# Kernel tuning notes

Hardware: AMD Instinct MI355X
Metric: run time of the kernel (lower is better)

## Reference

```python
import jax, jax.numpy as jnp
import numpy as np

SIGMA_INIT = 1000.0


def setup_inputs() -> dict:
    key = jax.random.key(0)
    k1, k2, k3 = jax.random.split(key, 3)
    B, M, D, S = 1024, 209, 12288, 2
    input_data = jax.random.normal(k1, (B, D), dtype=jnp.float32)
    center = jax.random.normal(k2, (M, D), dtype=jnp.float32)
    sigma = SIGMA_INIT * jnp.ones((M,), dtype=jnp.float32)
    W = 50.0 * jax.random.normal(k3, (S, M), dtype=jnp.float32)
    b = jnp.zeros((S,), dtype=jnp.float32)
    return {"input_data": input_data, "center": center, "sigma": sigma, "W": W, "b": b}


def reference(input_data, center, sigma, W, b):
    # Euclidean distance ||x_i - c_j|| via GEMM expansion (avoids [B,M,D] diff tensor)
    x2 = jnp.sum(input_data * input_data, axis=1, keepdims=True)        # [B,1]
    c2 = jnp.sum(center * center, axis=1)[None, :]                      # [1,M]
    d2 = x2 + c2 - 2.0 * (input_data @ center.T)                        # [B,M]
    dist = jnp.sqrt(jnp.maximum(d2, 0.0))
    # Note: original divides the (non-squared) norm by sigma^2, then exp(-.)
    radial = jnp.exp(-dist / (sigma * sigma)[None, :])                  # [B,M]
    return radial @ W.T + b                                             # [B,S]
```

## Files before the change

kernel.cpp:

```cpp
#include <hip/hip_runtime.h>
#include <hip/hip_bf16.h>
#include <stdint.h>

#define B_SZ 1024
#define M_SZ 209
#define D_SZ 12288
#define S_SZ 2

#define BT   64
#define MT   224
#define NCT  14
#define KC   48
#define KCH  (D_SZ / KC)
#define BK   64
#define NIT  (KCH / BK)
#define LDX  72

#define WS_DOT_OFF 1280

typedef __attribute__((ext_vector_type(8))) short short8;
typedef __attribute__((ext_vector_type(4))) float floatx4;

__device__ __forceinline__ uint32_t pk2(float lo, float hi) {
    union { __hip_bfloat162 h; uint32_t u; } cv;
    cv.h = __float22bfloat162_rn(float2{lo, hi});
    return cv.u;
}

__global__ __launch_bounds__(256, 3) void rbf_main(
    const float* __restrict__ x, const float* __restrict__ c,
    float* __restrict__ dot, float* __restrict__ xx, float* __restrict__ cc,
    int atomic_mode)
{
    __shared__ unsigned short sx[BT * LDX];
    __shared__ unsigned short sc[MT * LDX];

    const int t      = threadIdx.x;
    const int kchunk = blockIdx.x;
    const int bchunk = blockIdx.y;
    const int wave   = t >> 6;
    const int lane   = t & 63;
    const int quad   = lane >> 4;
    const int mrow   = lane & 15;

    floatx4 acc[NCT];
    const floatx4 zero4 = {0.f, 0.f, 0.f, 0.f};
#pragma unroll
    for (int i = 0; i < NCT; ++i) acc[i] = zero4;

    const int r     = t >> 2;
    const int cbase = (t & 3) * 16;

    const float* xp = x + (size_t)(bchunk * BT + r) * D_SZ + kchunk * KCH + cbase;
    const float* cp = c + (size_t)r * D_SZ + kchunk * KCH + cbase;
    const bool do_cc = (bchunk == 0);

    float sxx = 0.f;
    float scc[4] = {0.f, 0.f, 0.f, 0.f};

    for (int it = 0; it < NIT; ++it) {
        {
            float4 v0 = *(const float4*)(xp + 0);
            float4 v1 = *(const float4*)(xp + 4);
            float4 v2 = *(const float4*)(xp + 8);
            float4 v3 = *(const float4*)(xp + 12);
            sxx += v0.x*v0.x + v0.y*v0.y + v0.z*v0.z + v0.w*v0.w
                 + v1.x*v1.x + v1.y*v1.y + v1.z*v1.z + v1.w*v1.w
                 + v2.x*v2.x + v2.y*v2.y + v2.z*v2.z + v2.w*v2.w
                 + v3.x*v3.x + v3.y*v3.y + v3.z*v3.z + v3.w*v3.w;
            uint4 w0 = { pk2(v0.x,v0.y), pk2(v0.z,v0.w), pk2(v1.x,v1.y), pk2(v1.z,v1.w) };
            uint4 w1 = { pk2(v2.x,v2.y), pk2(v2.z,v2.w), pk2(v3.x,v3.y), pk2(v3.z,v3.w) };
            *(uint4*)(&sx[r * LDX + cbase])     = w0;
            *(uint4*)(&sx[r * LDX + cbase + 8]) = w1;
        }
#pragma unroll
        for (int rb = 0; rb < 4; ++rb) {
            const int crow = rb * 64 + r;
            if (rb < 3 || r < 32) {
                const bool valid = crow < M_SZ;
                const float* p = cp + (size_t)rb * 64 * D_SZ;
                float4 v0, v1, v2, v3;
                if (valid) {
                    v0 = *(const float4*)(p + 0);  v1 = *(const float4*)(p + 4);
                    v2 = *(const float4*)(p + 8);  v3 = *(const float4*)(p + 12);
                } else {
                    v0 = v1 = v2 = v3 = make_float4(0.f, 0.f, 0.f, 0.f);
                }
                if (do_cc && valid) {
                    scc[rb] += v0.x*v0.x + v0.y*v0.y + v0.z*v0.z + v0.w*v0.w
                             + v1.x*v1.x + v1.y*v1.y + v1.z*v1.z + v1.w*v1.w
                             + v2.x*v2.x + v2.y*v2.y + v2.z*v2.z + v2.w*v2.w
                             + v3.x*v3.x + v3.y*v3.y + v3.z*v3.z + v3.w*v3.w;
                }
                uint4 w0 = { pk2(v0.x,v0.y), pk2(v0.z,v0.w), pk2(v1.x,v1.y), pk2(v1.z,v1.w) };
                uint4 w1 = { pk2(v2.x,v2.y), pk2(v2.z,v2.w), pk2(v3.x,v3.y), pk2(v3.z,v3.w) };
                *(uint4*)(&sc[crow * LDX + cbase])     = w0;
                *(uint4*)(&sc[crow * LDX + cbase + 8]) = w1;
            }
        }
        __syncthreads();

        const unsigned short* ax = &sx[(wave * 16 + mrow) * LDX + quad * 8];
        const unsigned short* bx = &sc[mrow * LDX + quad * 8];
#pragma unroll
        for (int k0 = 0; k0 < BK; k0 += 32) {
            short8 a = *(const short8*)(ax + k0);
#pragma unroll
            for (int ct = 0; ct < NCT; ++ct) {
                short8 b = *(const short8*)(bx + ct * 16 * LDX + k0);
                acc[ct] = __builtin_amdgcn_mfma_f32_16x16x32_bf16(a, b, acc[ct], 0, 0, 0);
            }
        }
        __syncthreads();
        xp += BK;
        cp += BK;
    }

    float* dst = atomic_mode ? dot : dot + (size_t)kchunk * B_SZ * M_SZ;
    const int gi0 = bchunk * BT + wave * 16 + quad * 4;
#pragma unroll
    for (int ct = 0; ct < NCT; ++ct) {
        const int gj = ct * 16 + mrow;
        if (gj < M_SZ) {
#pragma unroll
            for (int rg = 0; rg < 4; ++rg) {
                const size_t idx = (size_t)(gi0 + rg) * M_SZ + gj;
                if (atomic_mode) atomicAdd(&dst[idx], acc[ct][rg]);
                else             dst[idx] = acc[ct][rg];
            }
        }
    }

    sxx += __shfl_down(sxx, 2);
    sxx += __shfl_down(sxx, 1);
    if ((t & 3) == 0) atomicAdd(&xx[bchunk * BT + r], sxx);

    if (do_cc) {
#pragma unroll
        for (int rb = 0; rb < 4; ++rb) {
            float s = scc[rb];
            s += __shfl_down(s, 2);
            s += __shfl_down(s, 1);
            const int crow = rb * 64 + r;
            if ((t & 3) == 0 && crow < M_SZ) atomicAdd(&cc[crow], s);
        }
    }
}

template <int NKC>
__global__ __launch_bounds__(256) void rbf_fin(
    const float* __restrict__ dot, const float* __restrict__ xx,
    const float* __restrict__ cc, const float* __restrict__ sigma,
    const float* __restrict__ W, const float* __restrict__ bias,
    float* __restrict__ out)
{
    const int wave = threadIdx.x >> 6, lane = threadIdx.x & 63;
    const int i = blockIdx.x * 4 + wave;
    const float xxi = xx[i];
    float a0 = 0.f, a1 = 0.f;
    for (int j = lane; j < M_SZ; j += 64) {
        float s = 0.f;
#pragma unroll
        for (int k = 0; k < NKC; ++k)
            s += dot[(size_t)k * B_SZ * M_SZ + (size_t)i * M_SZ + j];
        float d2 = fmaxf(xxi + cc[j] - 2.f * s, 0.f);
        float sg = sigma[j];
        float rad = __expf(-sqrtf(d2) / (sg * sg));
        a0 += rad * W[j];
        a1 += rad * W[M_SZ + j];
    }
#pragma unroll
    for (int off = 32; off > 0; off >>= 1) {
        a0 += __shfl_down(a0, off);
        a1 += __shfl_down(a1, off);
    }
    if (lane == 0) {
        out[i * 2 + 0] = a0 + bias[0];
        out[i * 2 + 1] = a1 + bias[1];
    }
}

extern "C" void kernel_launch(void* const* d_in, const int* in_sizes, int n_in,
                              void* d_out, int out_size, void* d_ws, size_t ws_size,
                              hipStream_t stream)
{
    const float* x     = (const float*)d_in[0];
    const float* c     = (const float*)d_in[1];
    const float* sigma = (const float*)d_in[2];
    const float* W     = (const float*)d_in[3];
    const float* bias  = (const float*)d_in[4];
    float* out = (float*)d_out;

    float* xx  = (float*)d_ws;
    float* cc  = xx + B_SZ;
    float* dot = (float*)d_ws + WS_DOT_OFF;

    const size_t slab_bytes = ((size_t)WS_DOT_OFF + (size_t)KC * B_SZ * M_SZ) * 4;
    const int atomic_mode = (ws_size < slab_bytes) ? 1 : 0;

    const size_t zero_bytes = atomic_mode
        ? ((size_t)WS_DOT_OFF + (size_t)B_SZ * M_SZ) * 4
        : (size_t)WS_DOT_OFF * 4;
    hipMemsetAsync(d_ws, 0, zero_bytes, stream);

    rbf_main<<<dim3(KC, B_SZ / BT), 256, 0, stream>>>(x, c, dot, xx, cc, atomic_mode);
    if (atomic_mode)
        rbf_fin<1><<<B_SZ / 4, 256, 0, stream>>>(dot, xx, cc, sigma, W, bias, out);
    else
        rbf_fin<KC><<<B_SZ / 4, 256, 0, stream>>>(dot, xx, cc, sigma, W, bias, out);
}
```

Measured before the change: 125.2 us.

## Split center dimension across a third grid axis to double block count

Each block now processes half the centers (112 instead of 224 padded), with a new grid z-dimension of 2, halving per-block accumulators and shared memory. Launch bounds are raised to 6 blocks per CU to exploit the lower register/LDS footprint and improve occupancy and latency hiding. The cost is that each x tile is loaded and converted twice (once per center half), increasing global traffic for x, while the squared-norm accumulation for x is restricted to the first half.

```diff
diff --git a/kernel.cpp b/kernel.cpp
--- a/kernel.cpp
+++ b/kernel.cpp
@@ -8,8 +8,9 @@
 #define S_SZ 2
 
 #define BT   64
-#define MT   224
-#define NCT  14
+#define MS   2
+#define MTH  112
+#define NCT  7
 #define KC   48
 #define KCH  (D_SZ / KC)
 #define BK   64
@@ -27,17 +28,26 @@
     return cv.u;
 }
 
-__global__ __launch_bounds__(256, 3) void rbf_main(
+__device__ __forceinline__ float sq16(const float4& a, const float4& b,
+                                      const float4& c, const float4& d) {
+    return a.x*a.x + a.y*a.y + a.z*a.z + a.w*a.w
+         + b.x*b.x + b.y*b.y + b.z*b.z + b.w*b.w
+         + c.x*c.x + c.y*c.y + c.z*c.z + c.w*c.w
+         + d.x*d.x + d.y*d.y + d.z*d.z + d.w*d.w;
+}
+
+__global__ __launch_bounds__(256, 6) void rbf_main(
     const float* __restrict__ x, const float* __restrict__ c,
     float* __restrict__ dot, float* __restrict__ xx, float* __restrict__ cc,
     int atomic_mode)
 {
     __shared__ unsigned short sx[BT * LDX];
-    __shared__ unsigned short sc[MT * LDX];
+    __shared__ unsigned short sc[MTH * LDX];
 
     const int t      = threadIdx.x;
     const int kchunk = blockIdx.x;
     const int bchunk = blockIdx.y;
+    const int mchunk = blockIdx.z;
     const int wave   = t >> 6;
     const int lane   = t & 63;
     const int quad   = lane >> 4;
@@ -51,12 +61,12 @@
     const int r     = t >> 2;
     const int cbase = (t & 3) * 16;
 
-    const float* xp = x + (size_t)(bchunk * BT + r) * D_SZ + kchunk * KCH + cbase;
-    const float* cp = c + (size_t)r * D_SZ + kchunk * KCH + cbase;
+    const float* xp  = x + (size_t)(bchunk * BT + r) * D_SZ + kchunk * KCH + cbase;
+    const float* cp0 = c + (size_t)mchunk * MTH * D_SZ + kchunk * KCH + cbase;
     const bool do_cc = (bchunk == 0);
 
     float sxx = 0.f;
-    float scc[4] = {0.f, 0.f, 0.f, 0.f};
+    float scc[2] = {0.f, 0.f};
 
     for (int it = 0; it < NIT; ++it) {
         {
@@ -64,21 +74,19 @@
             float4 v1 = *(const float4*)(xp + 4);
             float4 v2 = *(const float4*)(xp + 8);
             float4 v3 = *(const float4*)(xp + 12);
-            sxx += v0.x*v0.x + v0.y*v0.y + v0.z*v0.z + v0.w*v0.w
-                 + v1.x*v1.x + v1.y*v1.y + v1.z*v1.z + v1.w*v1.w
-                 + v2.x*v2.x + v2.y*v2.y + v2.z*v2.z + v2.w*v2.w
-                 + v3.x*v3.x + v3.y*v3.y + v3.z*v3.z + v3.w*v3.w;
+            sxx += sq16(v0, v1, v2, v3);
             uint4 w0 = { pk2(v0.x,v0.y), pk2(v0.z,v0.w), pk2(v1.x,v1.y), pk2(v1.z,v1.w) };
             uint4 w1 = { pk2(v2.x,v2.y), pk2(v2.z,v2.w), pk2(v3.x,v3.y), pk2(v3.z,v3.w) };
             *(uint4*)(&sx[r * LDX + cbase])     = w0;
             *(uint4*)(&sx[r * LDX + cbase + 8]) = w1;
         }
 #pragma unroll
-        for (int rb = 0; rb < 4; ++rb) {
+        for (int rb = 0; rb < 2; ++rb) {
             const int crow = rb * 64 + r;
-            if (rb < 3 || r < 32) {
-                const bool valid = crow < M_SZ;
-                const float* p = cp + (size_t)rb * 64 * D_SZ;
+            if (rb == 0 || r < 48) {
+                const int  grow  = mchunk * MTH + crow;
+                const bool valid = grow < M_SZ;
+                const float* p = cp0 + (size_t)crow * D_SZ;
                 float4 v0, v1, v2, v3;
                 if (valid) {
                     v0 = *(const float4*)(p + 0);  v1 = *(const float4*)(p + 4);
@@ -86,12 +94,7 @@
                 } else {
                     v0 = v1 = v2 = v3 = make_float4(0.f, 0.f, 0.f, 0.f);
                 }
-                if (do_cc && valid) {
-                    scc[rb] += v0.x*v0.x + v0.y*v0.y + v0.z*v0.z + v0.w*v0.w
-                             + v1.x*v1.x + v1.y*v1.y + v1.z*v1.z + v1.w*v1.w
-                             + v2.x*v2.x + v2.y*v2.y + v2.z*v2.z + v2.w*v2.w
-                             + v3.x*v3.x + v3.y*v3.y + v3.z*v3.z + v3.w*v3.w;
-                }
+                if (do_cc && valid) scc[rb] += sq16(v0, v1, v2, v3);
                 uint4 w0 = { pk2(v0.x,v0.y), pk2(v0.z,v0.w), pk2(v1.x,v1.y), pk2(v1.z,v1.w) };
                 uint4 w1 = { pk2(v2.x,v2.y), pk2(v2.z,v2.w), pk2(v3.x,v3.y), pk2(v3.z,v3.w) };
                 *(uint4*)(&sc[crow * LDX + cbase])     = w0;
@@ -113,14 +116,14 @@
         }
         __syncthreads();
         xp += BK;
-        cp += BK;
+        cp0 += BK;
     }
 
     float* dst = atomic_mode ? dot : dot + (size_t)kchunk * B_SZ * M_SZ;
     const int gi0 = bchunk * BT + wave * 16 + quad * 4;
 #pragma unroll
     for (int ct = 0; ct < NCT; ++ct) {
-        const int gj = ct * 16 + mrow;
+        const int gj = mchunk * MTH + ct * 16 + mrow;
         if (gj < M_SZ) {
 #pragma unroll
             for (int rg = 0; rg < 4; ++rg) {
@@ -131,18 +134,21 @@
         }
     }
 
-    sxx += __shfl_down(sxx, 2);
-    sxx += __shfl_down(sxx, 1);
-    if ((t & 3) == 0) atomicAdd(&xx[bchunk * BT + r], sxx);
+    if (mchunk == 0) {
+        sxx += __shfl_down(sxx, 2);
+        sxx += __shfl_down(sxx, 1);
+        if ((t & 3) == 0) atomicAdd(&xx[bchunk * BT + r], sxx);
+    }
 
     if (do_cc) {
 #pragma unroll
-        for (int rb = 0; rb < 4; ++rb) {
+        for (int rb = 0; rb < 2; ++rb) {
             float s = scc[rb];
             s += __shfl_down(s, 2);
             s += __shfl_down(s, 1);
-            const int crow = rb * 64 + r;
-            if ((t & 3) == 0 && crow < M_SZ) atomicAdd(&cc[crow], s);
+            const int grow = mchunk * MTH + rb * 64 + r;
+            if ((t & 3) == 0 && (rb == 0 || r < 48) && grow < M_SZ)
+                atomicAdd(&cc[grow], s);
         }
     }
 }
@@ -203,7 +209,7 @@
         : (size_t)WS_DOT_OFF * 4;
     hipMemsetAsync(d_ws, 0, zero_bytes, stream);
 
-    rbf_main<<<dim3(KC, B_SZ / BT), 256, 0, stream>>>(x, c, dot, xx, cc, atomic_mode);
+    rbf_main<<<dim3(KC, B_SZ / BT, MS), 256, 0, stream>>>(x, c, dot, xx, cc, atomic_mode);
     if (atomic_mode)
         rbf_fin<1><<<B_SZ / 4, 256, 0, stream>>>(dot, xx, cc, sigma, W, bias, out);
     else
```

Result: slower. 146.7 us (+17.2%).

## Pre-convert centers to bf16, async-load to swizzled LDS, store bf16 partials

Applied to the files above, without the earlier changes.

A new prep kernel converts the centers to a padded bf16 copy once and computes their squared norms. The main kernel then loads these tiles straight into LDS with global_load_lds, using an XOR-swizzled layout in place of padded rows to avoid bank conflicts. The per-K-chunk partial dot products are written as bf16 instead of fp32, and x norms go to per-chunk slots rather than atomics, which removes the memset and the atomic fallback path. This cuts the centers read per block, the fp32 convert work repeated across 16 batch chunks, and the slab write/read traffic. In exchange it adds a launch and loses accuracy by rounding partial sums to bf16 before the distance computation, which is large cancellation-sensitive.

```diff
diff --git a/kernel.cpp b/kernel.cpp
--- a/kernel.cpp
+++ b/kernel.cpp
@@ -4,19 +4,20 @@
 
 #define B_SZ 1024
 #define M_SZ 209
+#define MPAD 224
 #define D_SZ 12288
-#define S_SZ 2
-
-#define BT   64
-#define MT   224
-#define NCT  14
 #define KC   48
 #define KCH  (D_SZ / KC)
 #define BK   64
 #define NIT  (KCH / BK)
-#define LDX  72
-
-#define WS_DOT_OFF 1280
+#define NB   16
+#define BT   64
+#define NCT  14
+
+#define CBF_OFF  0u
+#define XXP_OFF  (MPAD * D_SZ * 2)
+#define CC_OFF   (XXP_OFF + B_SZ * KC * 4)
+#define SLAB_OFF (CC_OFF + 1024)
 
 typedef __attribute__((ext_vector_type(8))) short short8;
 typedef __attribute__((ext_vector_type(4))) float floatx4;
@@ -27,38 +28,81 @@
     return cv.u;
 }
 
+__device__ __forceinline__ void gload_lds16(const void* g, void* l) {
+    __builtin_amdgcn_global_load_lds(
+        (const __attribute__((address_space(1))) void*)g,
+        (__attribute__((address_space(3))) void*)l, 16, 0, 0);
+}
+
+__global__ __launch_bounds__(256) void rbf_prep(
+    const float* __restrict__ c, unsigned short* __restrict__ cbf,
+    float* __restrict__ cc)
+{
+    __shared__ float red[4];
+    const int j = blockIdx.x, t = threadIdx.x;
+    unsigned short* dst = cbf + (size_t)j * D_SZ;
+    float s = 0.f;
+    if (j < M_SZ) {
+        const float* src = c + (size_t)j * D_SZ;
+        for (int i = t * 4; i < D_SZ; i += 1024) {
+            float4 v = *(const float4*)(src + i);
+            s += v.x*v.x + v.y*v.y + v.z*v.z + v.w*v.w;
+            uint2 w = { pk2(v.x, v.y), pk2(v.z, v.w) };
+            *(uint2*)(dst + i) = w;
+        }
+    } else {
+        uint2 zz = {0u, 0u};
+        for (int i = t * 4; i < D_SZ; i += 1024) *(uint2*)(dst + i) = zz;
+    }
+#pragma unroll
+    for (int off = 32; off > 0; off >>= 1) s += __shfl_down(s, off);
+    if ((t & 63) == 0) red[t >> 6] = s;
+    __syncthreads();
+    if (t == 0 && j < M_SZ) cc[j] = red[0] + red[1] + red[2] + red[3];
+}
+
 __global__ __launch_bounds__(256, 3) void rbf_main(
-    const float* __restrict__ x, const float* __restrict__ c,
-    float* __restrict__ dot, float* __restrict__ xx, float* __restrict__ cc,
-    int atomic_mode)
-{
-    __shared__ unsigned short sx[BT * LDX];
-    __shared__ unsigned short sc[MT * LDX];
-
-    const int t      = threadIdx.x;
-    const int kchunk = blockIdx.x;
-    const int bchunk = blockIdx.y;
-    const int wave   = t >> 6;
-    const int lane   = t & 63;
-    const int quad   = lane >> 4;
-    const int mrow   = lane & 15;
+    const float* __restrict__ x, const unsigned short* __restrict__ cbf,
+    __hip_bfloat16* __restrict__ slab, float* __restrict__ xxp)
+{
+    __shared__ unsigned short sx[BT * BK];
+    __shared__ unsigned short sc[MPAD * BK];
+
+    const int t    = threadIdx.x;
+    const int k    = blockIdx.x;
+    const int b    = blockIdx.y;
+    const int wave = t >> 6, lane = t & 63;
+    const int quad = lane >> 4, mrow = lane & 15;
+    const int m3   = mrow & 7;
 
     floatx4 acc[NCT];
-    const floatx4 zero4 = {0.f, 0.f, 0.f, 0.f};
-#pragma unroll
-    for (int i = 0; i < NCT; ++i) acc[i] = zero4;
-
-    const int r     = t >> 2;
-    const int cbase = (t & 3) * 16;
-
-    const float* xp = x + (size_t)(bchunk * BT + r) * D_SZ + kchunk * KCH + cbase;
-    const float* cp = c + (size_t)r * D_SZ + kchunk * KCH + cbase;
-    const bool do_cc = (bchunk == 0);
+    const floatx4 z4 = {0.f, 0.f, 0.f, 0.f};
+#pragma unroll
+    for (int i = 0; i < NCT; ++i) acc[i] = z4;
+
+    const int r  = t >> 2;
+    const int c0 = (t & 3) * 2;
+    const float* xp = x + (size_t)(b * BT + r) * D_SZ + (size_t)k * KCH + (t & 3) * 16;
+    unsigned short* xw0 = &sx[r * BK + ((c0    ) ^ (r & 7)) * 8];
+    unsigned short* xw1 = &sx[r * BK + ((c0 + 1) ^ (r & 7)) * 8];
+
+    const int lr8 = lane >> 3, lc8 = lane & 7;
+    const unsigned short* cpb = cbf + (size_t)lr8 * D_SZ + (size_t)k * KCH
+                              + (size_t)((lc8 ^ lr8) * 8);
+
+    const unsigned short* ax0 = &sx[(wave * 16 + mrow) * BK + ((quad    ) ^ m3) * 8];
+    const unsigned short* ax1 = &sx[(wave * 16 + mrow) * BK + ((quad + 4) ^ m3) * 8];
+    const unsigned short* bx0 = &sc[mrow * BK + ((quad    ) ^ m3) * 8];
+    const unsigned short* bx1 = &sc[mrow * BK + ((quad + 4) ^ m3) * 8];
 
     float sxx = 0.f;
-    float scc[4] = {0.f, 0.f, 0.f, 0.f};
 
     for (int it = 0; it < NIT; ++it) {
+#pragma unroll
+        for (int j = 0; j < 7; ++j) {
+            const int cr = wave * 7 + j;
+            gload_lds16(cpb + (size_t)cr * 8 * D_SZ + it * BK, &sc[cr * 512]);
+        }
         {
             float4 v0 = *(const float4*)(xp + 0);
             float4 v1 = *(const float4*)(xp + 4);
@@ -70,99 +114,62 @@
                  + v3.x*v3.x + v3.y*v3.y + v3.z*v3.z + v3.w*v3.w;
             uint4 w0 = { pk2(v0.x,v0.y), pk2(v0.z,v0.w), pk2(v1.x,v1.y), pk2(v1.z,v1.w) };
             uint4 w1 = { pk2(v2.x,v2.y), pk2(v2.z,v2.w), pk2(v3.x,v3.y), pk2(v3.z,v3.w) };
-            *(uint4*)(&sx[r * LDX + cbase])     = w0;
-            *(uint4*)(&sx[r * LDX + cbase + 8]) = w1;
-        }
-#pragma unroll
-        for (int rb = 0; rb < 4; ++rb) {
-            const int crow = rb * 64 + r;
-            if (rb < 3 || r < 32) {
-                const bool valid = crow < M_SZ;
-                const float* p = cp + (size_t)rb * 64 * D_SZ;
-                float4 v0, v1, v2, v3;
-                if (valid) {
-                    v0 = *(const float4*)(p + 0);  v1 = *(const float4*)(p + 4);
-                    v2 = *(const float4*)(p + 8);  v3 = *(const float4*)(p + 12);
-                } else {
-                    v0 = v1 = v2 = v3 = make_float4(0.f, 0.f, 0.f, 0.f);
-                }
-                if (do_cc && valid) {
-                    scc[rb] += v0.x*v0.x + v0.y*v0.y + v0.z*v0.z + v0.w*v0.w
-                             + v1.x*v1.x + v1.y*v1.y + v1.z*v1.z + v1.w*v1.w
-                             + v2.x*v2.x + v2.y*v2.y + v2.z*v2.z + v2.w*v2.w
-                             + v3.x*v3.x + v3.y*v3.y + v3.z*v3.z + v3.w*v3.w;
-                }
-                uint4 w0 = { pk2(v0.x,v0.y), pk2(v0.z,v0.w), pk2(v1.x,v1.y), pk2(v1.z,v1.w) };
-                uint4 w1 = { pk2(v2.x,v2.y), pk2(v2.z,v2.w), pk2(v3.x,v3.y), pk2(v3.z,v3.w) };
-                *(uint4*)(&sc[crow * LDX + cbase])     = w0;
-                *(uint4*)(&sc[crow * LDX + cbase + 8]) = w1;
-            }
+            *(uint4*)xw0 = w0;
+            *(uint4*)xw1 = w1;
         }
         __syncthreads();
 
-        const unsigned short* ax = &sx[(wave * 16 + mrow) * LDX + quad * 8];
-        const unsigned short* bx = &sc[mrow * LDX + quad * 8];
-#pragma unroll
-        for (int k0 = 0; k0 < BK; k0 += 32) {
-            short8 a = *(const short8*)(ax + k0);
+#pragma unroll
+        for (int ks = 0; ks < 2; ++ks) {
+            short8 a = *(const short8*)(ks ? ax1 : ax0);
+            const unsigned short* bb = ks ? bx1 : bx0;
 #pragma unroll
             for (int ct = 0; ct < NCT; ++ct) {
-                short8 b = *(const short8*)(bx + ct * 16 * LDX + k0);
-                acc[ct] = __builtin_amdgcn_mfma_f32_16x16x32_bf16(a, b, acc[ct], 0, 0, 0);
+                short8 bf = *(const short8*)(bb + ct * 1024);
+                acc[ct] = __builtin_amdgcn_mfma_f32_16x16x32_bf16(a, bf, acc[ct], 0, 0, 0);
             }
         }
         __syncthreads();
         xp += BK;
-        cp += BK;
-    }
-
-    float* dst = atomic_mode ? dot : dot + (size_t)kchunk * B_SZ * M_SZ;
-    const int gi0 = bchunk * BT + wave * 16 + quad * 4;
+    }
+
+    __hip_bfloat16* sd = slab + (size_t)k * B_SZ * M_SZ;
+    const int gi0 = b * BT + wave * 16 + quad * 4;
 #pragma unroll
     for (int ct = 0; ct < NCT; ++ct) {
         const int gj = ct * 16 + mrow;
         if (gj < M_SZ) {
 #pragma unroll
-            for (int rg = 0; rg < 4; ++rg) {
-                const size_t idx = (size_t)(gi0 + rg) * M_SZ + gj;
-                if (atomic_mode) atomicAdd(&dst[idx], acc[ct][rg]);
-                else             dst[idx] = acc[ct][rg];
-            }
+            for (int rg = 0; rg < 4; ++rg)
+                sd[(size_t)(gi0 + rg) * M_SZ + gj] = __float2bfloat16(acc[ct][rg]);
         }
     }
 
     sxx += __shfl_down(sxx, 2);
     sxx += __shfl_down(sxx, 1);
-    if ((t & 3) == 0) atomicAdd(&xx[bchunk * BT + r], sxx);
-
-    if (do_cc) {
-#pragma unroll
-        for (int rb = 0; rb < 4; ++rb) {
-            float s = scc[rb];
-            s += __shfl_down(s, 2);
-            s += __shfl_down(s, 1);
-            const int crow = rb * 64 + r;
-            if ((t & 3) == 0 && crow < M_SZ) atomicAdd(&cc[crow], s);
-        }
-    }
-}
-
-template <int NKC>
+    if ((t & 3) == 0) xxp[(size_t)(b * BT + r) * KC + k] = sxx;
+}
+
 __global__ __launch_bounds__(256) void rbf_fin(
-    const float* __restrict__ dot, const float* __restrict__ xx,
+    const __hip_bfloat16* __restrict__ slab, const float* __restrict__ xxp,
     const float* __restrict__ cc, const float* __restrict__ sigma,
     const float* __restrict__ W, const float* __restrict__ bias,
     float* __restrict__ out)
 {
     const int wave = threadIdx.x >> 6, lane = threadIdx.x & 63;
     const int i = blockIdx.x * 4 + wave;
-    const float xxi = xx[i];
+
+    float xv = (lane < KC) ? xxp[(size_t)i * KC + lane] : 0.f;
+#pragma unroll
+    for (int off = 32; off > 0; off >>= 1) xv += __shfl_down(xv, off);
+    const float xxi = __shfl(xv, 0);
+
     float a0 = 0.f, a1 = 0.f;
     for (int j = lane; j < M_SZ; j += 64) {
         float s = 0.f;
 #pragma unroll
-        for (int k = 0; k < NKC; ++k)
-            s += dot[(size_t)k * B_SZ * M_SZ + (size_t)i * M_SZ + j];
+        for (int kk = 0; kk < KC; ++kk)
+            s += __bfloat162float(slab[(size_t)kk * B_SZ * M_SZ + (size_t)i * M_SZ + j]);
         float d2 = fmaxf(xxi + cc[j] - 2.f * s, 0.f);
         float sg = sigma[j];
         float rad = __expf(-sqrtf(d2) / (sg * sg));
@@ -191,21 +198,13 @@
     const float* bias  = (const float*)d_in[4];
     float* out = (float*)d_out;
 
-    float* xx  = (float*)d_ws;
-    float* cc  = xx + B_SZ;
-    float* dot = (float*)d_ws + WS_DOT_OFF;
-
-    const size_t slab_bytes = ((size_t)WS_DOT_OFF + (size_t)KC * B_SZ * M_SZ) * 4;
-    const int atomic_mode = (ws_size < slab_bytes) ? 1 : 0;
-
-    const size_t zero_bytes = atomic_mode
-        ? ((size_t)WS_DOT_OFF + (size_t)B_SZ * M_SZ) * 4
-        : (size_t)WS_DOT_OFF * 4;
-    hipMemsetAsync(d_ws, 0, zero_bytes, stream);
-
-    rbf_main<<<dim3(KC, B_SZ / BT), 256, 0, stream>>>(x, c, dot, xx, cc, atomic_mode);
-    if (atomic_mode)
-        rbf_fin<1><<<B_SZ / 4, 256, 0, stream>>>(dot, xx, cc, sigma, W, bias, out);
-    else
-        rbf_fin<KC><<<B_SZ / 4, 256, 0, stream>>>(dot, xx, cc, sigma, W, bias, out);
-}
+    char* ws = (char*)d_ws;
+    unsigned short*  cbf  = (unsigned short*)(ws + CBF_OFF);
+    float*           xxp  = (float*)(ws + XXP_OFF);
+    float*           cc   = (float*)(ws + CC_OFF);
+    __hip_bfloat16*  slab = (__hip_bfloat16*)(ws + SLAB_OFF);
+
+    rbf_prep<<<MPAD, 256, 0, stream>>>(c, cbf, cc);
+    rbf_main<<<dim3(KC, NB), 256, 0, stream>>>(x, cbf, slab, xxp);
+    rbf_fin<<<B_SZ / 4, 256, 0, stream>>>(slab, xxp, cc, sigma, W, bias, out);
+}
```

New measurement: 119.1 us. 1.05x faster.
